# Optimization experiments

Measured on AMD Instinct MI355X. Metric: run time of the kernel, lower is better.

## Reference

```python
import jax, jax.numpy as jnp
import numpy as np

K = 3          # kernel_size
PAD = K // 2   # unfold padding
BN_EPS = 1e-5


def _conv(x, w, dilation, pad):
    # x: [B,C,H,W], w: [O,I,kh,kw]
    return jax.lax.conv_general_dilated(
        x, w, window_strides=(1, 1), padding=[(pad, pad), (pad, pad)],
        rhs_dilation=(dilation, dilation),
        dimension_numbers=("NCHW", "OIHW", "NCHW"))


def _bn(x, g, b, rm, rv):
    # eval-mode batchnorm with running stats
    inv = g / jnp.sqrt(rv + BN_EPS)
    return x * inv[None, :, None, None] + (b - rm * inv)[None, :, None, None]


def setup_inputs() -> dict:
    key = jax.random.key(0)
    ks = jax.random.split(key, 8)
    B, T, H, W = 8, 5, 512, 512
    mid = 16  # max(16, T // 4)
    inp = {
        "x_aligned": jax.random.normal(ks[0], (B, T, H, W), jnp.float32),
        "raw_diff": jax.random.normal(ks[1], (B, T - 1, H, W), jnp.float32),
        "w1": jax.random.normal(ks[2], (mid, T, 3, 3), jnp.float32) * 0.1,
        "g1": jnp.ones((mid,), jnp.float32), "b1": jnp.zeros((mid,), jnp.float32),
        "rm1": jnp.zeros((mid,), jnp.float32), "rv1": jnp.ones((mid,), jnp.float32),
        "w2": jax.random.normal(ks[3], (mid, mid, 3, 3), jnp.float32) * 0.1,
        "g2": jnp.ones((mid,), jnp.float32), "b2": jnp.zeros((mid,), jnp.float32),
        "rm2": jnp.zeros((mid,), jnp.float32), "rv2": jnp.ones((mid,), jnp.float32),
        "w3": jax.random.normal(ks[4], (mid, mid, 3, 3), jnp.float32) * 0.1,
        "g3": jnp.ones((mid,), jnp.float32), "b3": jnp.zeros((mid,), jnp.float32),
        "rm3": jnp.zeros((mid,), jnp.float32), "rv3": jnp.ones((mid,), jnp.float32),
        "w4": jax.random.normal(ks[5], (T * K * K, mid, 1, 1), jnp.float32) * 0.1,
        "bias": jnp.full((1,), -1.0, jnp.float32),
    }
    return inp


def reference(x_aligned, raw_diff, w1, g1, b1, rm1, rv1, w2, g2, b2, rm2, rv2,
              w3, g3, b3, rm3, rv3, w4, bias):
    B, T, H, W = x_aligned.shape
    # _accumulate: sequential abs-add == sum of abs over frame-diff axis
    acc = jnp.sum(jnp.abs(raw_diff), axis=1, keepdims=True)  # [B,1,H,W]
    mean = jnp.mean(acc)
    n = acc.size
    std = jnp.sqrt(jnp.sum((acc - mean) ** 2) / (n - 1))  # unbiased (torch default)
    motion = (acc - mean) / (std + 1e-6)
    motion_seq = jnp.broadcast_to(motion, (B, T, H, W))
    # _generate_kernel: conv+BN+ReLU stack with dilations 1,2,4 then 1x1
    h = jax.nn.relu(_bn(_conv(motion_seq, w1, 1, 1), g1, b1, rm1, rv1))
    h = jax.nn.relu(_bn(_conv(h, w2, 2, 2), g2, b2, rm2, rv2))
    h = jax.nn.relu(_bn(_conv(h, w3, 4, 4), g3, b3, rm3, rv3))
    raw_kernel = _conv(h, w4, 1, 0).reshape(B, T, K * K, H, W)
    kernel = (jax.nn.sigmoid(raw_kernel + bias[0]) + 0.01) * 10.0
    # _enhance: unfold (KxK patches, zero pad) then per-pixel weighted sum
    xp = jnp.pad(x_aligned, ((0, 0), (0, 0), (PAD, PAD), (PAD, PAD)))
    patches = jnp.stack(
        [xp[:, :, i:i + H, j:j + W] for i in range(K) for j in range(K)],
        axis=2)  # [B,T,K*K,H,W], matches F.unfold row-major kernel order
    return jnp.sum(kernel * patches, axis=2)  # [B,T,H,W]
```

## Files before the change

### kernel.cpp

```cpp
#include <hip/hip_runtime.h>
#include <hip/hip_bf16.h>
#include <math.h>

#define HH 512
#define WW 512
#define BB 8
#define TT 5
#define MID 16
#define HWSZ (HH*WW)
#define NPIX (BB*HWSZ)

typedef __attribute__((ext_vector_type(8))) short bf16x8;
typedef __attribute__((ext_vector_type(4))) float f32x4;

__device__ inline unsigned short f2bf(float f){
  unsigned u = __float_as_uint(f);
  u = u + 0x7fffu + ((u >> 16) & 1u);
  return (unsigned short)(u >> 16);
}
__device__ inline unsigned packpair(float a, float b){
  unsigned ua = __float_as_uint(a) + 0x8000u;
  unsigned ub = __float_as_uint(b) + 0x8000u;
  return __builtin_amdgcn_perm(ub, ua, 0x07060302u);
}
__device__ inline float blo(unsigned u){ return __uint_as_float(u << 16); }
__device__ inline float bhi(unsigned u){ return __uint_as_float(u & 0xffff0000u); }

union U4B { uint4 u; bf16x8 h; };


__global__ __launch_bounds__(256) void k_acc(const float* __restrict__ rd,
                                             float4* __restrict__ acc,
                                             float2* __restrict__ partial){
  int t = blockIdx.x * 256 + threadIdx.x;
  int i = t << 2;
  int b = i >> 18, p = i & (HWSZ - 1);
  const float* base = rd + (size_t)b * 4 * HWSZ + p;
  float4 f0 = *(const float4*)(base);
  float4 f1 = *(const float4*)(base + HWSZ);
  float4 f2 = *(const float4*)(base + 2*HWSZ);
  float4 f3 = *(const float4*)(base + 3*HWSZ);
  float4 s4;
  s4.x = fabsf(f0.x) + fabsf(f1.x) + fabsf(f2.x) + fabsf(f3.x);
  s4.y = fabsf(f0.y) + fabsf(f1.y) + fabsf(f2.y) + fabsf(f3.y);
  s4.z = fabsf(f0.z) + fabsf(f1.z) + fabsf(f2.z) + fabsf(f3.z);
  s4.w = fabsf(f0.w) + fabsf(f1.w) + fabsf(f2.w) + fabsf(f3.w);
  acc[t] = s4;
  float s  = s4.x + s4.y + s4.z + s4.w;
  float s2 = s4.x*s4.x + s4.y*s4.y + s4.z*s4.z + s4.w*s4.w;
  #pragma unroll
  for (int off = 32; off; off >>= 1){
    s  += __shfl_down(s,  off);
    s2 += __shfl_down(s2, off);
  }
  __shared__ float ls[4], ls2[4];
  int lane = threadIdx.x & 63, wid = threadIdx.x >> 6;
  if (lane == 0){ ls[wid] = s; ls2[wid] = s2; }
  __syncthreads();
  if (threadIdx.x == 0)
    partial[blockIdx.x] = make_float2(ls[0]+ls[1]+ls[2]+ls[3],
                                      ls2[0]+ls2[1]+ls2[2]+ls2[3]);
}

__global__ __launch_bounds__(256) void k_prep(const float2* __restrict__ partial,
    const float* __restrict__ w1, const float* __restrict__ w2, const float* __restrict__ w3,
    const float* __restrict__ g1, const float* __restrict__ b1, const float* __restrict__ rm1, const float* __restrict__ rv1,
    const float* __restrict__ g2, const float* __restrict__ b2, const float* __restrict__ rm2, const float* __restrict__ rv2,
    const float* __restrict__ g3, const float* __restrict__ b3, const float* __restrict__ rm3, const float* __restrict__ rv3,
    const float* __restrict__ w4, const float* __restrict__ bias0,
    float* __restrict__ cst, unsigned* __restrict__ wsB2, unsigned* __restrict__ wsB3,
    uint4* __restrict__ wsB4){
  int t = threadIdx.x;
  double s = 0.0, s2 = 0.0;
  for (int j = t; j < 2048; j += 256){
    float2 v = partial[j];
    s += (double)v.x; s2 += (double)v.y;
  }
  #pragma unroll
  for (int off = 32; off; off >>= 1){
    s  += __shfl_down(s,  off);
    s2 += __shfl_down(s2, off);
  }
  __shared__ double ds[4], ds2[4];
  int lane = t & 63, wid = t >> 6;
  if (lane == 0){ ds[wid] = s; ds2[wid] = s2; }
  __syncthreads();
  if (t == 0){
    double S  = ds[0]+ds[1]+ds[2]+ds[3];
    double S2 = ds2[0]+ds2[1]+ds2[2]+ds2[3];
    double n = (double)NPIX;
    double mean = S / n;
    double var  = (S2 - n * mean * mean) / (n - 1.0);
    double sd   = sqrt(var);
    cst[0] = (float)mean;
    cst[1] = (float)(1.0 / (sd + 1e-6));
    cst[242] = bias0[0];
  }
  if (t < 144){
    int c = t / 9, k = t % 9;
    float sw = 0.f;
    for (int f = 0; f < TT; f++) sw += w1[c*45 + f*9 + k];
    cst[2 + t] = sw;
  }
  if (t < 16){
    float s1 = g1[t] * rsqrtf(rv1[t] + 1e-5f);
    cst[146 + t] = s1; cst[162 + t] = b1[t] - rm1[t] * s1;
    float c2 = g2[t] * rsqrtf(rv2[t] + 1e-5f);
    cst[288 + t] = c2; cst[304 + t] = b2[t] - rm2[t] * c2;
    float c3 = g3[t] * rsqrtf(rv3[t] + 1e-5f);
    cst[320 + t] = c3; cst[336 + t] = b3[t] - rm3[t] * c3;
  }
  for (int it = 0; it < 5; it++){
    int idx = it * 256 + t;
    int m = idx >> 8, rem = idx & 255;
    int L = rem >> 2, jj = rem & 3;
    int out = L & 15, q = L >> 4;
    unsigned v2 = 0, v3 = 0;
    #pragma unroll
    for (int h = 0; h < 2; h++){
      int j = 2*jj + h;
      int k = q*8 + j;
      int tap = 2*m + (k >> 4);
      int ci = k & 15;
      unsigned bv2 = 0, bv3 = 0;
      if (tap < 9){
        bv2 = f2bf(w2[out*144 + ci*9 + tap]);
        bv3 = f2bf(w3[out*144 + ci*9 + tap]);
      }
      v2 |= bv2 << (16*h);
      v3 |= bv3 << (16*h);
    }
    wsB2[idx] = v2; wsB3[idx] = v3;
  }
  if (t < 192){
    int c = t >> 6, L = t & 63;
    int n = L & 15, q = L >> 4;
    int o = c*16 + n;
    unsigned vv[4];
    #pragma unroll
    for (int jj = 0; jj < 4; jj++){
      unsigned pk = 0;
      #pragma unroll
      for (int h = 0; h < 2; h++){
        int j = 2*jj + h, kci = q*8 + j;
        unsigned bv = 0;
        if (kci < 16 && o < 45) bv = f2bf(w4[o*16 + kci]);
        pk |= bv << (16*h);
      }
      vv[jj] = pk;
    }
    wsB4[c*64 + L] = make_uint4(vv[0], vv[1], vv[2], vv[3]);
  }
}

#define TR 12
#define TC 68
__global__ __launch_bounds__(256) void k_conv12(const float* __restrict__ acc,
                                                const float* __restrict__ C,
                                                const unsigned* __restrict__ wsB2,
                                                uint2* __restrict__ h2){
  __shared__ float AT[14*72];
  __shared__ uint4 PL[2][TR*TC];
  int tid = threadIdx.x;
  int blk = blockIdx.x;
  int xt = blk & 7, yt = (blk >> 3) & 63, b = blk >> 9;
  int y0 = yt << 3, x0 = xt << 6;
  float mean = C[0], inv = C[1];
  const float* ab = acc + ((size_t)b << 18);
  #pragma unroll
  for (int it = 0; it < 4; it++){
    int idx = it*256 + tid;
    if (idx < 14*72){
      int r = (idx * 1821) >> 17;
      int p = idx - r*72;
      int gy = y0 - 3 + r, gx = x0 - 3 + p;
      float v = 0.f;
      if ((unsigned)gy < HH && (unsigned)gx < WW)
        v = (ab[(gy << 9) + gx] - mean) * inv;
      AT[idx] = v;
    }
  }
  __syncthreads();
  #pragma unroll
  for (int it = 0; it < 4; it++){
    int i = it*256 + tid;
    if (i < TR*TC){
      int r2 = (i * 241) >> 14;
      int p2 = i - r2*TC;
      int gy = y0 - 2 + r2, gx = x0 - 2 + p2;
      uint4 lo = make_uint4(0u,0u,0u,0u), hi = lo;
      if ((unsigned)gy < HH && (unsigned)gx < WW){
        float a[MID];
        #pragma unroll
        for (int o = 0; o < MID; o++) a[o] = 0.f;
        #pragma unroll
        for (int ky = 0; ky < 3; ky++){
          #pragma unroll
          for (int kx = 0; kx < 3; kx++){
            float m = AT[(r2 + ky)*72 + (p2 + kx)];
            int k = ky * 3 + kx;
            #pragma unroll
            for (int o = 0; o < MID; o++) a[o] = fmaf(C[2 + o*9 + k], m, a[o]);
          }
        }
        unsigned pk[8];
        #pragma unroll
        for (int j = 0; j < 8; j++){
          float v0 = fmaxf(0.f, fmaf(a[2*j],   C[146 + 2*j],   C[162 + 2*j]));
          float v1 = fmaxf(0.f, fmaf(a[2*j+1], C[146 + 2*j+1], C[162 + 2*j+1]));
          pk[j] = packpair(v0, v1);
        }
        lo = make_uint4(pk[0], pk[1], pk[2], pk[3]);
        hi = make_uint4(pk[4], pk[5], pk[6], pk[7]);
      }
      PL[0][r2*TC + p2] = lo;
      PL[1][r2*TC + p2] = hi;
    }
  }
  __syncthreads();
  int lane = tid & 63, wv = tid >> 6;
  int col = lane & 15, q = lane >> 4;
  int chSel = q & 1;
  bool hiTap = (q >= 2);
  uint4 wfrag[5];
  #pragma unroll
  for (int m = 0; m < 5; m++) wfrag[m] = ((const uint4*)wsB2)[m*64 + lane];
  float4 sc = *(const float4*)&C[288 + q*4];
  float4 bi = *(const float4*)&C[304 + q*4];
  #pragma unroll
  for (int rr = 0; rr < 2; rr++){
    int ly = wv*2 + rr;
    #pragma unroll
    for (int g = 0; g < 4; g++){
      int lx = g << 4;
      f32x4 cc = {0.f, 0.f, 0.f, 0.f};
      #pragma unroll
      for (int m = 0; m < 5; m++){
        const int ta = 2*m, tb = (2*m + 1 > 8) ? 8 : (2*m + 1);
        int dy = (hiTap ? tb/3 : ta/3) - 1;
        int dx = (hiTap ? tb%3 : ta%3) - 1;
        int trow = ly + 2 + 2*dy;
        int tpx  = lx + 2 + col + 2*dx;
        U4B bv; bv.u = PL[chSel][trow*TC + tpx];
        U4B wb; wb.u = wfrag[m];
        cc = __builtin_amdgcn_mfma_f32_16x16x32_bf16(wb.h, bv.h, cc, 0, 0, 0);
      }
      float v0 = fmaxf(0.f, fmaf(cc[0], sc.x, bi.x));
      float v1 = fmaxf(0.f, fmaf(cc[1], sc.y, bi.y));
      float v2 = fmaxf(0.f, fmaf(cc[2], sc.z, bi.z));
      float v3 = fmaxf(0.f, fmaf(cc[3], sc.w, bi.w));
      int gy = y0 + ly, gx = x0 + lx + col;
      h2[(size_t)((b << 18) | (gy << 9) | gx)*4 + q] =
          make_uint2(packpair(v0, v1), packpair(v2, v3));
    }
  }
}

template<bool EDGE>
__device__ inline f32x4 convW4(const uint4* __restrict__ hin, const uint4 wfrag[5],
                               int b, int y, int x0, int col, int q, f32x4 cc){
  int chSel = q & 1;
  bool hiTap = (q >= 2);
  #pragma unroll
  for (int m = 0; m < 5; m++){
    const int ta = 2*m, tb = (2*m + 1 > 8) ? 8 : (2*m + 1);
    int dy = (hiTap ? tb/3 : ta/3) - 1;
    int dx = (hiTap ? tb%3 : ta%3) - 1;
    int yy = y + dy * 4;
    int xx = x0 + col + dx * 4;
    U4B a;
    if (EDGE){
      bool valid = ((unsigned)yy < HH) && ((unsigned)xx < WW);
      a.u = make_uint4(0u, 0u, 0u, 0u);
      if (valid) a.u = hin[(((unsigned)((b << 18) | (yy << 9) | xx)) << 1) | (unsigned)chSel];
    } else {
      a.u = hin[(((unsigned)((b << 18) | (yy << 9) | xx)) << 1) | (unsigned)chSel];
    }
    U4B bb; bb.u = wfrag[m];
    cc = __builtin_amdgcn_mfma_f32_16x16x32_bf16(bb.h, a.h, cc, 0, 0, 0);
  }
  return cc;
}

__global__ __launch_bounds__(256) void k_conv3m(const uint4* __restrict__ h2,
                                                const float* __restrict__ C,
                                                const unsigned* __restrict__ wsB3,
                                                const uint4* __restrict__ wsB4,
                                                const float* __restrict__ xal,
                                                float* __restrict__ out){
  __shared__ uint2 LB[4][832];
  int lane = threadIdx.x & 63, wv = threadIdx.x >> 6;
  char* myL = (char*)LB[wv];
  unsigned short* Lk = (unsigned short*)myL;
  int w = blockIdx.x * 4 + wv;
  int base = w << 6;
  int b = base >> 18, rem = base & (HWSZ - 1);
  int y = rem >> 9, wx = rem & 511;
  uint4 wfrag[5];
  #pragma unroll
  for (int m = 0; m < 5; m++) wfrag[m] = ((const uint4*)wsB3)[m*64 + lane];
  uint4 bw[3];
  #pragma unroll
  for (int c = 0; c < 3; c++) bw[c] = wsB4[c*64 + lane];
  int col = lane & 15, q = lane >> 4;
  float4 sc = *(const float4*)&C[320 + q*4];
  float4 bi = *(const float4*)&C[336 + q*4];
  float cb = C[242];
  int src0 = col + q*32;
  int src1 = src0 + 16;
  bool yIn = (y >= 4) && (y < 508);

  #pragma unroll
  for (int g = 0; g < 4; g++){
    int x0 = wx + g*16;
    f32x4 cc = {0.f, 0.f, 0.f, 0.f};
    bool fast = yIn && (x0 >= 4) && (x0 <= 492);
    if (fast) cc = convW4<false>(h2, wfrag, b, y, x0, col, q, cc);
    else      cc = convW4<true >(h2, wfrag, b, y, x0, col, q, cc);
    float v0 = fmaxf(0.f, fmaf(cc[0], sc.x, bi.x));
    float v1 = fmaxf(0.f, fmaf(cc[1], sc.y, bi.y));
    float v2 = fmaxf(0.f, fmaf(cc[2], sc.z, bi.z));
    float v3 = fmaxf(0.f, fmaf(cc[3], sc.w, bi.w));
    int pk01 = (int)packpair(v0, v1);
    int pk23 = (int)packpair(v2, v3);

    U4B a;
    a.u.x = (unsigned)__shfl(pk01, src0);
    a.u.y = (unsigned)__shfl(pk23, src0);
    a.u.z = (unsigned)__shfl(pk01, src1);
    a.u.w = (unsigned)__shfl(pk23, src1);

    #pragma unroll
    for (int c = 0; c < 3; c++){
      f32x4 aw = {cb, cb, cb, cb};
      U4B bb; bb.u = bw[c];
      aw = __builtin_amdgcn_mfma_f32_16x16x32_bf16(a.h, bb.h, aw, 0, 0, 0);
      #pragma unroll
      for (int r = 0; r < 4; r++){
        float e  = __expf(-aw[r]);
        float rc = __builtin_amdgcn_rcpf(1.f + e);
        float kern = fmaf(10.f, rc, 0.1f);
        unsigned u = __float_as_uint(kern) + 0x8000u;
        Lk[(g*16 + q*4 + r)*52 + c*16 + col] = (unsigned short)(u >> 16);
      }
    }
  }

  unsigned kvf[24];
  {
    const uint2* kp = (const uint2*)(myL + lane*104);
    #pragma unroll
    for (int jj = 0; jj < 12; jj++){
      uint2 u = kp[jj];
      kvf[2*jj] = u.x; kvf[2*jj+1] = u.y;
    }
  }
  int px = wx + lane;
  bool mxl = (px > 0), mxr = (px < 511), mym = (y > 0), myp = (y < 511);
  bool msk[9] = { mym&&mxl, mym, mym&&mxr,
                  mxl,      true, mxr,
                  myp&&mxl, myp, myp&&mxr };
  int rowm = mym ? -2048 : 0;
  int rowp = myp ?  2048 : 0;
  int loff = mxl ? -4 : 0;
  int roff = mxr ?  4 : 0;
  const char* base0 = (const char*)(xal + ((size_t)(b*TT) << 18) + (y << 9) + px);
  #pragma unroll
  for (int t = 0; t < TT; t++){
    const char* pc = base0 + (size_t)t * (HWSZ*4);
    const char* pm = pc + rowm;
    const char* pp = pc + rowp;
    float xv[9];
    xv[0] = *(const float*)(pm + loff);
    xv[1] = *(const float*)(pm);
    xv[2] = *(const float*)(pm + roff);
    xv[3] = *(const float*)(pc + loff);
    xv[4] = *(const float*)(pc);
    xv[5] = *(const float*)(pc + roff);
    xv[6] = *(const float*)(pp + loff);
    xv[7] = *(const float*)(pp);
    xv[8] = *(const float*)(pp + roff);
    float ov = 0.f;
    #pragma unroll
    for (int k = 0; k < 9; k++){
      int n = t*9 + k;
      unsigned u = kvf[n >> 1];
      float kf = (n & 1) ? bhi(u) : blo(u);
      float kern = msk[k] ? kf : 0.f;
      ov = fmaf(kern, xv[k], ov);
    }
    out[((size_t)(b*TT + t) << 18) + (y << 9) + px] = ov;
  }
}

extern "C" void kernel_launch(void* const* d_in, const int* in_sizes, int n_in,
                              void* d_out, int out_size, void* d_ws, size_t ws_size,
                              hipStream_t stream){
  const float* xal = (const float*)d_in[0];
  const float* rd  = (const float*)d_in[1];
  const float* w1  = (const float*)d_in[2];
  const float* g1  = (const float*)d_in[3];
  const float* b1  = (const float*)d_in[4];
  const float* rm1 = (const float*)d_in[5];
  const float* rv1 = (const float*)d_in[6];
  const float* w2  = (const float*)d_in[7];
  const float* g2  = (const float*)d_in[8];
  const float* b2  = (const float*)d_in[9];
  const float* rm2 = (const float*)d_in[10];
  const float* rv2 = (const float*)d_in[11];
  const float* w3  = (const float*)d_in[12];
  const float* g3  = (const float*)d_in[13];
  const float* b3  = (const float*)d_in[14];
  const float* rm3 = (const float*)d_in[15];
  const float* rv3 = (const float*)d_in[16];
  const float* w4  = (const float*)d_in[17];
  const float* bias= (const float*)d_in[18];
  float* out = (float*)d_out;

  char* ws = (char*)d_ws;
  float2*   partial = (float2*)ws;
  float*    cst   = (float*)(ws + 16384);
  unsigned* wsB2  = (unsigned*)(ws + 32768);
  unsigned* wsB3  = (unsigned*)(ws + 40960);
  uint4*    wsB4  = (uint4*)(ws + 49152);
  float*    acc   = (float*)(ws + 65536);
  char*     h2    = (char*)(ws + 65536 + (size_t)NPIX*4);

  k_acc<<<2048, 256, 0, stream>>>(rd, (float4*)acc, partial);
  k_prep<<<1, 256, 0, stream>>>(partial, w1, w2, w3,
                                g1, b1, rm1, rv1,
                                g2, b2, rm2, rv2,
                                g3, b3, rm3, rv3, w4, bias, cst, wsB2, wsB3, wsB4);
  k_conv12<<<4096, 256, 0, stream>>>(acc, cst, wsB2, (uint2*)h2);
  k_conv3m<<<NPIX/256, 256, 0, stream>>>((const uint4*)h2, cst, wsB3, wsB4, xal, out);
}
```

Baseline: 252.7 us.

## Split conv3 pixel groups and output frames across waves in a block

Before, each wave in k_conv3m handled 64 pixels on its own: it ran four conv3 MFMA groups, then computed all five output frames. Now a block covers 64 pixels. Each wave computes one 16-pixel conv3/1x1/sigmoid group into shared memory, then after __syncthreads the waves split the per-frame enhance work. The grid grows fourfold so the serial per-wave chain is shorter and there is more parallelism to hide latency. In exchange it adds a block barrier, and wave 0 handles two of the five frames, which leaves the enhance phase unevenly loaded.

Result: slower. 271.1 us (+7.3%).

```diff
diff --git a/kernel.cpp b/kernel.cpp
--- a/kernel.cpp
+++ b/kernel.cpp
@@ -288,73 +288,60 @@
                                                 const uint4* __restrict__ wsB4,
                                                 const float* __restrict__ xal,
                                                 float* __restrict__ out){
-  __shared__ uint2 LB[4][832];
-  int lane = threadIdx.x & 63, wv = threadIdx.x >> 6;
-  char* myL = (char*)LB[wv];
-  unsigned short* Lk = (unsigned short*)myL;
-  int w = blockIdx.x * 4 + wv;
-  int base = w << 6;
+  __shared__ unsigned LkU[64*26];
+  unsigned short* Lk = (unsigned short*)LkU;
+  int tid = threadIdx.x;
+  int lane = tid & 63, wv = tid >> 6;
+  int base = blockIdx.x << 6;
   int b = base >> 18, rem = base & (HWSZ - 1);
   int y = rem >> 9, wx = rem & 511;
+  int col = lane & 15, q = lane >> 4;
   uint4 wfrag[5];
   #pragma unroll
   for (int m = 0; m < 5; m++) wfrag[m] = ((const uint4*)wsB3)[m*64 + lane];
   uint4 bw[3];
   #pragma unroll
   for (int c = 0; c < 3; c++) bw[c] = wsB4[c*64 + lane];
-  int col = lane & 15, q = lane >> 4;
   float4 sc = *(const float4*)&C[320 + q*4];
   float4 bi = *(const float4*)&C[336 + q*4];
   float cb = C[242];
   int src0 = col + q*32;
   int src1 = src0 + 16;
-  bool yIn = (y >= 4) && (y < 508);
-
-  #pragma unroll
-  for (int g = 0; g < 4; g++){
-    int x0 = wx + g*16;
-    f32x4 cc = {0.f, 0.f, 0.f, 0.f};
-    bool fast = yIn && (x0 >= 4) && (x0 <= 492);
-    if (fast) cc = convW4<false>(h2, wfrag, b, y, x0, col, q, cc);
-    else      cc = convW4<true >(h2, wfrag, b, y, x0, col, q, cc);
-    float v0 = fmaxf(0.f, fmaf(cc[0], sc.x, bi.x));
-    float v1 = fmaxf(0.f, fmaf(cc[1], sc.y, bi.y));
-    float v2 = fmaxf(0.f, fmaf(cc[2], sc.z, bi.z));
-    float v3 = fmaxf(0.f, fmaf(cc[3], sc.w, bi.w));
-    int pk01 = (int)packpair(v0, v1);
-    int pk23 = (int)packpair(v2, v3);
-
-    U4B a;
-    a.u.x = (unsigned)__shfl(pk01, src0);
-    a.u.y = (unsigned)__shfl(pk23, src0);
-    a.u.z = (unsigned)__shfl(pk01, src1);
-    a.u.w = (unsigned)__shfl(pk23, src1);
-
-    #pragma unroll
-    for (int c = 0; c < 3; c++){
-      f32x4 aw = {cb, cb, cb, cb};
-      U4B bb; bb.u = bw[c];
-      aw = __builtin_amdgcn_mfma_f32_16x16x32_bf16(a.h, bb.h, aw, 0, 0, 0);
-      #pragma unroll
-      for (int r = 0; r < 4; r++){
-        float e  = __expf(-aw[r]);
-        float rc = __builtin_amdgcn_rcpf(1.f + e);
-        float kern = fmaf(10.f, rc, 0.1f);
-        unsigned u = __float_as_uint(kern) + 0x8000u;
-        Lk[(g*16 + q*4 + r)*52 + c*16 + col] = (unsigned short)(u >> 16);
-      }
-    }
-  }
-
-  unsigned kvf[24];
-  {
-    const uint2* kp = (const uint2*)(myL + lane*104);
-    #pragma unroll
-    for (int jj = 0; jj < 12; jj++){
-      uint2 u = kp[jj];
-      kvf[2*jj] = u.x; kvf[2*jj+1] = u.y;
-    }
-  }
+
+  int x0 = wx + (wv << 4);
+  bool fast = (y >= 4) && (y < 508) && (x0 >= 4) && (x0 <= 492);
+  f32x4 cc = {0.f, 0.f, 0.f, 0.f};
+  if (fast) cc = convW4<false>(h2, wfrag, b, y, x0, col, q, cc);
+  else      cc = convW4<true >(h2, wfrag, b, y, x0, col, q, cc);
+  float v0 = fmaxf(0.f, fmaf(cc[0], sc.x, bi.x));
+  float v1 = fmaxf(0.f, fmaf(cc[1], sc.y, bi.y));
+  float v2 = fmaxf(0.f, fmaf(cc[2], sc.z, bi.z));
+  float v3 = fmaxf(0.f, fmaf(cc[3], sc.w, bi.w));
+  int pk01 = (int)packpair(v0, v1);
+  int pk23 = (int)packpair(v2, v3);
+
+  U4B a;
+  a.u.x = (unsigned)__shfl(pk01, src0);
+  a.u.y = (unsigned)__shfl(pk23, src0);
+  a.u.z = (unsigned)__shfl(pk01, src1);
+  a.u.w = (unsigned)__shfl(pk23, src1);
+
+  #pragma unroll
+  for (int c = 0; c < 3; c++){
+    f32x4 aw = {cb, cb, cb, cb};
+    U4B bb; bb.u = bw[c];
+    aw = __builtin_amdgcn_mfma_f32_16x16x32_bf16(a.h, bb.h, aw, 0, 0, 0);
+    #pragma unroll
+    for (int r = 0; r < 4; r++){
+      float e  = __expf(-aw[r]);
+      float rc = __builtin_amdgcn_rcpf(1.f + e);
+      float kern = fmaf(10.f, rc, 0.1f);
+      unsigned u = __float_as_uint(kern) + 0x8000u;
+      Lk[((wv << 4) + q*4 + r)*52 + c*16 + col] = (unsigned short)(u >> 16);
+    }
+  }
+  __syncthreads();
+
   int px = wx + lane;
   bool mxl = (px > 0), mxr = (px < 511), mym = (y > 0), myp = (y < 511);
   bool msk[9] = { mym&&mxl, mym, mym&&mxr,
@@ -366,7 +353,13 @@
   int roff = mxr ?  4 : 0;
   const char* base0 = (const char*)(xal + ((size_t)(b*TT) << 18) + (y << 9) + px);
   #pragma unroll
-  for (int t = 0; t < TT; t++){
+  for (int rep = 0; rep < 2; rep++){
+    int t = (rep == 0) ? wv : 4;
+    if (rep == 1 && wv != 0) break;
+    int d0 = (t*9) >> 1, off = (t*9) & 1;
+    unsigned kv[6];
+    #pragma unroll
+    for (int j = 0; j < 6; j++) kv[j] = LkU[lane*26 + d0 + j];
     const char* pc = base0 + (size_t)t * (HWSZ*4);
     const char* pm = pc + rowm;
     const char* pp = pc + rowp;
@@ -383,9 +376,9 @@
     float ov = 0.f;
     #pragma unroll
     for (int k = 0; k < 9; k++){
-      int n = t*9 + k;
-      unsigned u = kvf[n >> 1];
-      float kf = (n & 1) ? bhi(u) : blo(u);
+      int nrel = off + k;
+      unsigned u = kv[nrel >> 1];
+      float kf = (nrel & 1) ? bhi(u) : blo(u);
       float kern = msk[k] ? kf : 0.f;
       ov = fmaf(kern, xv[k], ov);
     }
@@ -432,5 +425,5 @@
                                 g2, b2, rm2, rv2,
                                 g3, b3, rm3, rv3, w4, bias, cst, wsB2, wsB3, wsB4);
   k_conv12<<<4096, 256, 0, stream>>>(acc, cst, wsB2, (uint2*)h2);
-  k_conv3m<<<NPIX/256, 256, 0, stream>>>((const uint4*)h2, cst, wsB3, wsB4, xal, out);
-}
+  k_conv3m<<<NPIX/64, 256, 0, stream>>>((const uint4*)h2, cst, wsB3, wsB4, xal, out);
+}
```
